# Kernel tuning notes

Measured on AMD Instinct MI355X. Metric: run time of the kernel, lower is better.

The kernel has to match this reference:

```python
import jax, jax.numpy as jnp
import numpy as np

N = 100000
E = 1600000
D_IN = 128
HEADS = 4
C = 16  # hidden // heads
NEG_SLOPE = 0.2


def setup_inputs() -> dict:
    key = jax.random.key(0)
    ks = jax.random.split(key, 8)
    x = jax.random.normal(ks[0], (N, D_IN), dtype=jnp.float32)
    edge_index = jax.random.randint(ks[1], (2, E), 0, N, dtype=jnp.int32)
    s = 1.0 / np.sqrt(D_IN)
    W_l = jax.random.normal(ks[2], (D_IN, HEADS * C), dtype=jnp.float32) * s
    b_l = jnp.zeros((HEADS * C,), dtype=jnp.float32)
    W_r = jax.random.normal(ks[3], (D_IN, HEADS * C), dtype=jnp.float32) * s
    b_r = jnp.zeros((HEADS * C,), dtype=jnp.float32)
    att = jax.random.normal(ks[4], (HEADS, C), dtype=jnp.float32) * (1.0 / np.sqrt(C))
    bias = jnp.zeros((HEADS * C,), dtype=jnp.float32)
    W_head = jax.random.normal(ks[5], (HEADS * C, 1), dtype=jnp.float32) * (1.0 / np.sqrt(HEADS * C))
    b_head = jnp.zeros((1,), dtype=jnp.float32)
    return {"x": x, "edge_index": edge_index, "W_l": W_l, "b_l": b_l,
            "W_r": W_r, "b_r": b_r, "att": att, "bias": bias,
            "W_head": W_head, "b_head": b_head}


def reference(x, edge_index, W_l, b_l, W_r, b_r, att, bias, W_head, b_head):
    # GATv2Conv (PyG semantics, add_self_loops=True, concat=True)
    n = x.shape[0]
    # add self loops
    loops = jnp.arange(n, dtype=edge_index.dtype)
    src = jnp.concatenate([edge_index[0], loops])  # source j
    dst = jnp.concatenate([edge_index[1], loops])  # target i
    # per-node linear projections -> [N, H, C]
    x_l = (x @ W_l + b_l).reshape(n, HEADS, C)
    x_r = (x @ W_r + b_r).reshape(n, HEADS, C)
    # per-edge attention logits: att . LeakyReLU(x_l[j] + x_r[i])
    e = x_l[src] + x_r[dst]                               # [E', H, C]
    e = jnp.where(e >= 0, e, NEG_SLOPE * e)
    logits = jnp.einsum('ehc,hc->eh', e, att)             # [E', H]
    # segment softmax over incoming edges of each target node
    seg_max = jax.ops.segment_max(logits, dst, num_segments=n)  # [N, H]
    expw = jnp.exp(logits - seg_max[dst])
    seg_sum = jax.ops.segment_sum(expw, dst, num_segments=n)
    alpha = expw / seg_sum[dst]                           # [E', H]
    # weighted scatter-aggregate of source messages
    msg = alpha[:, :, None] * x_l[src]                    # [E', H, C]
    out = jax.ops.segment_sum(msg, dst, num_segments=n)   # [N, H, C]
    out = out.reshape(n, HEADS * C) + bias
    # ReLU + Linear head
    h = jax.nn.relu(out)
    return (h @ W_head + b_head).squeeze(-1)              # [N]
```

## Files before the change

### kernel.cpp

```cpp
#include <hip/hip_runtime.h>
#include <hip/hip_bf16.h>
#include <hip/hip_fp16.h>

#define HC 64
#define D_IN 128
#define NEG_SLOPE 0.2f
#define BCAP 8192

using f32x4 = __attribute__((ext_vector_type(4))) float;
using f16x8 = __attribute__((ext_vector_type(8))) _Float16;
using f16x2 = __attribute__((ext_vector_type(2))) _Float16;

__global__ void k_iota(int* __restrict__ p, int n) {
    int i = blockIdx.x * blockDim.x + threadIdx.x;
    if (i < n) p[i] = i * BCAP;
}

__global__ __launch_bounds__(256, 3) void k_proj(
    const float* __restrict__ x,
    const float* __restrict__ Wl, const float* __restrict__ bl,
    const float* __restrict__ Wr, const float* __restrict__ br,
    __half* __restrict__ xlh, float* __restrict__ xr, int N) {
    __shared__ _Float16 sWT[128 * 136];
    const int t = threadIdx.x;
    for (int idx = t; idx < 8192; idx += 256) {
        const int k = idx >> 6;
        const int c = idx & 63;
        sWT[c * 136 + k]        = (_Float16)Wl[idx];
        sWT[(c + 64) * 136 + k] = (_Float16)Wr[idx];
    }
    const int lane = t & 63;
    const int wave = t >> 6;
    const int m = lane & 15;
    const int q = lane >> 4;
    float bfu[8];
#pragma unroll
    for (int ct = 0; ct < 4; ++ct) bfu[ct] = bl[ct * 16 + m];
#pragma unroll
    for (int ct = 0; ct < 4; ++ct) bfu[4 + ct] = br[ct * 16 + m];
    __syncthreads();

    const int ntrip = N >> 5;
    for (int trip = blockIdx.x * 4 + wave; trip < ntrip; trip += gridDim.x * 4) {
        const int i0 = trip << 5;
        f16x8 af[2][4];
#pragma unroll
        for (int tt = 0; tt < 2; ++tt) {
            const float* xrow = x + (size_t)(i0 + tt * 16 + m) * D_IN + q * 8;
#pragma unroll
            for (int kk = 0; kk < 4; ++kk) {
                const float4* p4 = (const float4*)(xrow + kk * 32);
                float4 u = p4[0];
                float4 v = p4[1];
                f16x8 a;
                a[0] = (_Float16)u.x; a[1] = (_Float16)u.y;
                a[2] = (_Float16)u.z; a[3] = (_Float16)u.w;
                a[4] = (_Float16)v.x; a[5] = (_Float16)v.y;
                a[6] = (_Float16)v.z; a[7] = (_Float16)v.w;
                af[tt][kk] = a;
            }
        }
#pragma unroll
        for (int ct = 0; ct < 8; ++ct) {
            const _Float16* bp = &sWT[(ct * 16 + m) * 136 + q * 8];
            f32x4 acc0 = {0.f, 0.f, 0.f, 0.f};
            f32x4 acc1 = {0.f, 0.f, 0.f, 0.f};
#pragma unroll
            for (int kk = 0; kk < 4; ++kk) {
                f16x8 bf = *(const f16x8*)(bp + kk * 32);
                acc0 = __builtin_amdgcn_mfma_f32_16x16x32_f16(af[0][kk], bf, acc0, 0, 0, 0);
                acc1 = __builtin_amdgcn_mfma_f32_16x16x32_f16(af[1][kk], bf, acc1, 0, 0, 0);
            }
            const float bv = bfu[ct];
            if (ct < 4) {
                const int ch = ct * 16 + m;
#pragma unroll
                for (int r = 0; r < 4; ++r) {
                    xlh[(size_t)(i0 + q * 4 + r) * HC + ch]      = __float2half(acc0[r] + bv);
                    xlh[(size_t)(i0 + 16 + q * 4 + r) * HC + ch] = __float2half(acc1[r] + bv);
                }
            } else {
                const int ch = (ct - 4) * 16 + m;
#pragma unroll
                for (int r = 0; r < 4; ++r) {
                    xr[(size_t)(i0 + q * 4 + r) * HC + ch]      = acc0[r] + bv;
                    xr[(size_t)(i0 + 16 + q * 4 + r) * HC + ch] = acc1[r] + bv;
                }
            }
        }
    }
}

__global__ __launch_bounds__(256) void k_scat1(const int* __restrict__ src,
                                               const int* __restrict__ dst, int E,
                                               int* __restrict__ bfill,
                                               unsigned* __restrict__ coarse) {
    __shared__ int h[512], bl[512], cur[512];
    for (int t = threadIdx.x; t < 512; t += 256) { h[t] = 0; cur[t] = 0; }
    __syncthreads();
    const int beg = blockIdx.x * 8192;
    const int end = min(beg + 8192, E);
    for (int p = beg + threadIdx.x; p < end; p += 256)
        atomicAdd(&h[dst[p] >> 8], 1);
    __syncthreads();
    for (int t = threadIdx.x; t < 512; t += 256)
        bl[t] = h[t] ? atomicAdd(&bfill[t], h[t]) : 0;
    __syncthreads();
    for (int p = beg + threadIdx.x; p < end; p += 256) {
        const int d = dst[p];
        const int bin = d >> 8;
        const int r = atomicAdd(&cur[bin], 1);
        coarse[bl[bin] + r] = ((unsigned)src[p] << 8) | (unsigned)(d & 255);
    }
}

__global__ __launch_bounds__(256) void k_sort2(const unsigned* __restrict__ coarse,
                                               const int* __restrict__ bfill,
                                               int* __restrict__ row_off,
                                               int* __restrict__ endo,
                                               int* __restrict__ sorted_src, int N) {
    __shared__ int cnt[256], lds[256];
    const int t = threadIdx.x;
    const int b = blockIdx.x;
    const int eb = b * BCAP;
    const int ee = bfill[b];
    cnt[t] = 0;
    __syncthreads();
    for (int p = eb + t; p < ee; p += 256)
        atomicAdd(&cnt[coarse[p] & 255], 1);
    __syncthreads();
    const int c = cnt[t];
    lds[t] = c;
    __syncthreads();
    for (int o = 1; o < 256; o <<= 1) {
        int v = (t >= o) ? lds[t - o] : 0;
        __syncthreads();
        lds[t] += v;
        __syncthreads();
    }
    const int ex = lds[t] - c;
    const int node = (b << 8) + t;
    if (node < N) {
        row_off[node] = eb + ex;
        endo[node]    = eb + ex + c;
    }
    __syncthreads();
    cnt[t] = ex;
    __syncthreads();
    for (int p = eb + t; p < ee; p += 256) {
        const unsigned e = coarse[p];
        const int r = atomicAdd(&cnt[e & 255], 1);
        sorted_src[eb + r] = (int)(e >> 8);
    }
}

__device__ __forceinline__ float redquad(float v) {
    int a;
    a = __builtin_amdgcn_update_dpp(0, __float_as_int(v), 0xB1, 0xF, 0xF, true);
    v += __int_as_float(a);
    a = __builtin_amdgcn_update_dpp(0, __float_as_int(v), 0x4E, 0xF, 0xF, true);
    v += __int_as_float(a);
    return v;
}

__global__ __launch_bounds__(256) void k_agg(
    const __half* __restrict__ xlh, const float* __restrict__ xr,
    const float* __restrict__ att, const float* __restrict__ bias,
    const float* __restrict__ Wh, const float* __restrict__ bh,
    const int* __restrict__ row_off, const int* __restrict__ endo,
    const int* __restrict__ sorted_src, float* __restrict__ out, int N) {
    const int wave = threadIdx.x >> 6;
    const int lane = threadIdx.x & 63;
    const int i = blockIdx.x * 4 + wave;
    if (i >= N) return;
    const int sl   = lane & 15;
    const int slot = lane >> 4;

    const _Float16* xlhp = (const _Float16*)xlh;
    const float4 attf = *(const float4*)(att + 4 * sl);
    f16x2 attA, attB;
    attA[0] = (_Float16)(attf.x * 1.44269504f);
    attA[1] = (_Float16)(attf.y * 1.44269504f);
    attB[0] = (_Float16)(attf.z * 1.44269504f);
    attB[1] = (_Float16)(attf.w * 1.44269504f);
    const f16x2 c02 = {(_Float16)NEG_SLOPE, (_Float16)NEG_SLOPE};

    const float4 xrf = *(const float4*)(xr + ((size_t)i << 6) + 4 * sl);
    f16x2 xriA, xriB;
    xriA[0] = (_Float16)xrf.x; xriA[1] = (_Float16)xrf.y;
    xriB[0] = (_Float16)xrf.z; xriB[1] = (_Float16)xrf.w;
    const uint2 xliraw = *(const uint2*)(xlhp + ((size_t)i << 6) + 4 * sl);
    const f16x2 xliA = __builtin_bit_cast(f16x2, xliraw.x);
    const f16x2 xliB = __builtin_bit_cast(f16x2, xliraw.y);

    f16x2 vA = xliA + xriA, vB = xliB + xriB;
    vA = __builtin_elementwise_max(vA, vA * c02);
    vB = __builtin_elementwise_max(vB, vB * c02);
    float t0 = redquad(__builtin_amdgcn_fdot2(attB, vB,
                        __builtin_amdgcn_fdot2(attA, vA, 0.f, false), false));
    float pe0 = (slot == 0) ? exp2f(t0) : 0.f;
    float s  = pe0;
    float a0 = pe0 * (float)xliA[0];
    float a1 = pe0 * (float)xliA[1];
    float a2 = pe0 * (float)xliB[0];
    float a3 = pe0 * (float)xliB[1];

    int p = row_off[i];
    const int end = endo[i];

#define EDGE_GROUP(JEXPR, PRED)                                              \
    {                                                                        \
        int jj = (JEXPR);                                                    \
        uint2 raw = *(const uint2*)(xlhp + ((size_t)jj << 6) + 4 * sl);      \
        f16x2 xA = __builtin_bit_cast(f16x2, raw.x);                         \
        f16x2 xB = __builtin_bit_cast(f16x2, raw.y);                         \
        f16x2 wA = xA + xriA, wB = xB + xriB;                                \
        wA = __builtin_elementwise_max(wA, wA * c02);                        \
        wB = __builtin_elementwise_max(wB, wB * c02);                        \
        float tt = redquad(__builtin_amdgcn_fdot2(attB, wB,                  \
                     __builtin_amdgcn_fdot2(attA, wA, 0.f, false), false));  \
        float pe = (PRED) ? exp2f(tt) : 0.f;                                 \
        s += pe;                                                             \
        a0 = fmaf(pe, (float)xA[0], a0);                                     \
        a1 = fmaf(pe, (float)xA[1], a1);                                     \
        a2 = fmaf(pe, (float)xB[0], a2);                                     \
        a3 = fmaf(pe, (float)xB[1], a3);                                     \
    }

    for (; p + 8 <= end; p += 8) {
        int j0 = sorted_src[p + slot];
        int j1 = sorted_src[p + 4 + slot];
        EDGE_GROUP(j0, true)
        EDGE_GROUP(j1, true)
    }
    if (p + 4 <= end) {
        int j0 = sorted_src[p + slot];
        EDGE_GROUP(j0, true)
        p += 4;
    }
    const int rem = end - p;
    if (rem > 0) {
        int idx = p + slot;
        int j0 = sorted_src[(idx < end) ? idx : (end - 1)];
        EDGE_GROUP(j0, slot < rem)
    }
#undef EDGE_GROUP

    s  += __shfl_xor(s, 16);  s  += __shfl_xor(s, 32);
    a0 += __shfl_xor(a0, 16); a0 += __shfl_xor(a0, 32);
    a1 += __shfl_xor(a1, 16); a1 += __shfl_xor(a1, 32);
    a2 += __shfl_xor(a2, 16); a2 += __shfl_xor(a2, 32);
    a3 += __shfl_xor(a3, 16); a3 += __shfl_xor(a3, 32);

    const float4 bi = *(const float4*)(bias + 4 * sl);
    const float4 wh = *(const float4*)(Wh + 4 * sl);
    float y = fmaxf(a0 / s + bi.x, 0.f) * wh.x
            + fmaxf(a1 / s + bi.y, 0.f) * wh.y
            + fmaxf(a2 / s + bi.z, 0.f) * wh.z
            + fmaxf(a3 / s + bi.w, 0.f) * wh.w;
    y += __shfl_xor(y, 1);
    y += __shfl_xor(y, 2);
    y += __shfl_xor(y, 4);
    y += __shfl_xor(y, 8);
    if (lane == 0) out[i] = y + bh[0];
}

extern "C" void kernel_launch(void* const* d_in, const int* in_sizes, int n_in,
                              void* d_out, int out_size, void* d_ws, size_t ws_size,
                              hipStream_t stream) {
    const float* x   = (const float*)d_in[0];
    const int*   ei  = (const int*)d_in[1];
    const float* Wl  = (const float*)d_in[2];
    const float* bl  = (const float*)d_in[3];
    const float* Wr  = (const float*)d_in[4];
    const float* br  = (const float*)d_in[5];
    const float* att = (const float*)d_in[6];
    const float* bias= (const float*)d_in[7];
    const float* Wh  = (const float*)d_in[8];
    const float* bh  = (const float*)d_in[9];
    float* out = (float*)d_out;

    const int N = in_sizes[0] / D_IN;
    const int E = in_sizes[1] / 2;
    const int* src = ei;
    const int* dst = ei + E;
    const int nbkt = (N + 255) / 256;

    auto align = [](size_t v) { return (v + 255) & ~(size_t)255; };
    char* ws = (char*)d_ws;
    size_t off = 0;
    __half* xlh     = (__half*)(ws + off);   off = align(off + (size_t)N * HC * 2);
    float* xr       = (float*)(ws + off);    off = align(off + (size_t)N * HC * 4);
    int*   row_off  = (int*)(ws + off);      off = align(off + (size_t)N * 4);
    int*   endo     = (int*)(ws + off);      off = align(off + (size_t)N * 4);
    int*   bfill    = (int*)(ws + off);      off = align(off + 512 * 4);
    int*   sorted   = (int*)(ws + off);      off = align(off + (size_t)nbkt * BCAP * 4);
    unsigned* coarse= (unsigned*)(ws + off); off = align(off + (size_t)nbkt * BCAP * 4);
    (void)ws_size;

    k_iota<<<2, 256, 0, stream>>>(bfill, 512);

    k_proj<<<782, 256, 0, stream>>>(x, Wl, bl, Wr, br, xlh, xr, N);

    k_scat1<<<(E + 8191) / 8192, 256, 0, stream>>>(src, dst, E, bfill, coarse);
    k_sort2<<<nbkt, 256, 0, stream>>>(coarse, bfill, row_off, endo, sorted, N);

    k_agg<<<(N + 3) / 4, 256, 0, stream>>>(xlh, xr, att, bias, Wh, bh,
                                           row_off, endo, sorted, out, N);
}
```

Baseline: 229.7 us.

## Stage x tiles in LDS for projection, widen agg lanes to 8 channels

The projection kernel now stages a 32-row tile of x into LDS, converted to fp16, once per block, and splits the 8 output column tiles across the 4 waves. Before, each wave loaded its own rows and computed all 8 column tiles. In the aggregation kernel each lane now handles 8 channels with one 16-byte gather, so 8 edges are processed in parallel per wave instead of 4, and the per-edge reduction drops to a single DPP step. The scatter chunk size and the projection grid size also change. These trade extra block-level barriers and more registers per lane for wider memory accesses and more edge parallelism.

```diff
diff --git a/kernel.cpp b/kernel.cpp
--- a/kernel.cpp
+++ b/kernel.cpp
@@ -6,6 +6,7 @@
 #define D_IN 128
 #define NEG_SLOPE 0.2f
 #define BCAP 8192
+#define L2E 1.44269504f
 
 using f32x4 = __attribute__((ext_vector_type(4))) float;
 using f16x8 = __attribute__((ext_vector_type(8))) _Float16;
@@ -22,6 +23,7 @@
     const float* __restrict__ Wr, const float* __restrict__ br,
     __half* __restrict__ xlh, float* __restrict__ xr, int N) {
     __shared__ _Float16 sWT[128 * 136];
+    __shared__ _Float16 sX[32 * 136];
     const int t = threadIdx.x;
     for (int idx = t; idx < 8192; idx += 256) {
         const int k = idx >> 6;
@@ -33,35 +35,35 @@
     const int wave = t >> 6;
     const int m = lane & 15;
     const int q = lane >> 4;
-    float bfu[8];
-#pragma unroll
-    for (int ct = 0; ct < 4; ++ct) bfu[ct] = bl[ct * 16 + m];
-#pragma unroll
-    for (int ct = 0; ct < 4; ++ct) bfu[4 + ct] = br[ct * 16 + m];
+    float bfu[2];
+#pragma unroll
+    for (int cc = 0; cc < 2; ++cc) {
+        const int ct = wave * 2 + cc;
+        const int ch = (ct & 3) * 16 + m;
+        bfu[cc] = (ct < 4) ? bl[ch] : br[ch];
+    }
     __syncthreads();
 
     const int ntrip = N >> 5;
-    for (int trip = blockIdx.x * 4 + wave; trip < ntrip; trip += gridDim.x * 4) {
+    for (int trip = blockIdx.x; trip < ntrip; trip += gridDim.x) {
         const int i0 = trip << 5;
+        for (int c = t; c < 1024; c += 256) {
+            const int r = c >> 5, c4 = c & 31;
+            float4 v = ((const float4*)(x + (size_t)(i0 + r) * D_IN))[c4];
+            _Float16* dp = &sX[r * 136 + c4 * 4];
+            dp[0] = (_Float16)v.x; dp[1] = (_Float16)v.y;
+            dp[2] = (_Float16)v.z; dp[3] = (_Float16)v.w;
+        }
+        __syncthreads();
         f16x8 af[2][4];
 #pragma unroll
-        for (int tt = 0; tt < 2; ++tt) {
-            const float* xrow = x + (size_t)(i0 + tt * 16 + m) * D_IN + q * 8;
-#pragma unroll
-            for (int kk = 0; kk < 4; ++kk) {
-                const float4* p4 = (const float4*)(xrow + kk * 32);
-                float4 u = p4[0];
-                float4 v = p4[1];
-                f16x8 a;
-                a[0] = (_Float16)u.x; a[1] = (_Float16)u.y;
-                a[2] = (_Float16)u.z; a[3] = (_Float16)u.w;
-                a[4] = (_Float16)v.x; a[5] = (_Float16)v.y;
-                a[6] = (_Float16)v.z; a[7] = (_Float16)v.w;
-                af[tt][kk] = a;
-            }
-        }
-#pragma unroll
-        for (int ct = 0; ct < 8; ++ct) {
+        for (int tt = 0; tt < 2; ++tt)
+#pragma unroll
+            for (int kk = 0; kk < 4; ++kk)
+                af[tt][kk] = *(const f16x8*)&sX[(tt * 16 + m) * 136 + kk * 32 + q * 8];
+#pragma unroll
+        for (int cc = 0; cc < 2; ++cc) {
+            const int ct = wave * 2 + cc;
             const _Float16* bp = &sWT[(ct * 16 + m) * 136 + q * 8];
             f32x4 acc0 = {0.f, 0.f, 0.f, 0.f};
             f32x4 acc1 = {0.f, 0.f, 0.f, 0.f};
@@ -71,7 +73,7 @@
                 acc0 = __builtin_amdgcn_mfma_f32_16x16x32_f16(af[0][kk], bf, acc0, 0, 0, 0);
                 acc1 = __builtin_amdgcn_mfma_f32_16x16x32_f16(af[1][kk], bf, acc1, 0, 0, 0);
             }
-            const float bv = bfu[ct];
+            const float bv = bfu[cc];
             if (ct < 4) {
                 const int ch = ct * 16 + m;
 #pragma unroll
@@ -88,6 +90,7 @@
                 }
             }
         }
+        __syncthreads();
     }
 }
 
@@ -98,8 +101,8 @@
     __shared__ int h[512], bl[512], cur[512];
     for (int t = threadIdx.x; t < 512; t += 256) { h[t] = 0; cur[t] = 0; }
     __syncthreads();
-    const int beg = blockIdx.x * 8192;
-    const int end = min(beg + 8192, E);
+    const int beg = blockIdx.x * 4096;
+    const int end = min(beg + 4096, E);
     for (int p = beg + threadIdx.x; p < end; p += 256)
         atomicAdd(&h[dst[p] >> 8], 1);
     __syncthreads();
@@ -154,13 +157,9 @@
     }
 }
 
-__device__ __forceinline__ float redquad(float v) {
-    int a;
-    a = __builtin_amdgcn_update_dpp(0, __float_as_int(v), 0xB1, 0xF, 0xF, true);
-    v += __int_as_float(a);
-    a = __builtin_amdgcn_update_dpp(0, __float_as_int(v), 0x4E, 0xF, 0xF, true);
-    v += __int_as_float(a);
-    return v;
+__device__ __forceinline__ float redpair(float v) {
+    int a = __builtin_amdgcn_update_dpp(0, __float_as_int(v), 0xB1, 0xF, 0xF, true);
+    return v + __int_as_float(a);
 }
 
 __global__ __launch_bounds__(256) void k_agg(
@@ -173,95 +172,123 @@
     const int lane = threadIdx.x & 63;
     const int i = blockIdx.x * 4 + wave;
     if (i >= N) return;
-    const int sl   = lane & 15;
-    const int slot = lane >> 4;
+    const int sub  = lane & 7;
+    const int slot = lane >> 3;
 
     const _Float16* xlhp = (const _Float16*)xlh;
-    const float4 attf = *(const float4*)(att + 4 * sl);
-    f16x2 attA, attB;
-    attA[0] = (_Float16)(attf.x * 1.44269504f);
-    attA[1] = (_Float16)(attf.y * 1.44269504f);
-    attB[0] = (_Float16)(attf.z * 1.44269504f);
-    attB[1] = (_Float16)(attf.w * 1.44269504f);
+    const float4 atA = *(const float4*)(att + 8 * sub);
+    const float4 atB = *(const float4*)(att + 8 * sub + 4);
+    f16x2 at[4];
+    at[0][0] = (_Float16)(atA.x * L2E); at[0][1] = (_Float16)(atA.y * L2E);
+    at[1][0] = (_Float16)(atA.z * L2E); at[1][1] = (_Float16)(atA.w * L2E);
+    at[2][0] = (_Float16)(atB.x * L2E); at[2][1] = (_Float16)(atB.y * L2E);
+    at[3][0] = (_Float16)(atB.z * L2E); at[3][1] = (_Float16)(atB.w * L2E);
     const f16x2 c02 = {(_Float16)NEG_SLOPE, (_Float16)NEG_SLOPE};
 
-    const float4 xrf = *(const float4*)(xr + ((size_t)i << 6) + 4 * sl);
-    f16x2 xriA, xriB;
-    xriA[0] = (_Float16)xrf.x; xriA[1] = (_Float16)xrf.y;
-    xriB[0] = (_Float16)xrf.z; xriB[1] = (_Float16)xrf.w;
-    const uint2 xliraw = *(const uint2*)(xlhp + ((size_t)i << 6) + 4 * sl);
-    const f16x2 xliA = __builtin_bit_cast(f16x2, xliraw.x);
-    const f16x2 xliB = __builtin_bit_cast(f16x2, xliraw.y);
-
-    f16x2 vA = xliA + xriA, vB = xliB + xriB;
-    vA = __builtin_elementwise_max(vA, vA * c02);
-    vB = __builtin_elementwise_max(vB, vB * c02);
-    float t0 = redquad(__builtin_amdgcn_fdot2(attB, vB,
-                        __builtin_amdgcn_fdot2(attA, vA, 0.f, false), false));
-    float pe0 = (slot == 0) ? exp2f(t0) : 0.f;
-    float s  = pe0;
-    float a0 = pe0 * (float)xliA[0];
-    float a1 = pe0 * (float)xliA[1];
-    float a2 = pe0 * (float)xliB[0];
-    float a3 = pe0 * (float)xliB[1];
+    const float4 xrA = *(const float4*)(xr + ((size_t)i << 6) + 8 * sub);
+    const float4 xrB = *(const float4*)(xr + ((size_t)i << 6) + 8 * sub + 4);
+    f16x2 xri[4];
+    xri[0][0] = (_Float16)xrA.x; xri[0][1] = (_Float16)xrA.y;
+    xri[1][0] = (_Float16)xrA.z; xri[1][1] = (_Float16)xrA.w;
+    xri[2][0] = (_Float16)xrB.x; xri[2][1] = (_Float16)xrB.y;
+    xri[3][0] = (_Float16)xrB.z; xri[3][1] = (_Float16)xrB.w;
+
+    const uint4 xliraw = *(const uint4*)(xlhp + ((size_t)i << 6) + 8 * sub);
+    f16x2 xli[4];
+    xli[0] = __builtin_bit_cast(f16x2, xliraw.x);
+    xli[1] = __builtin_bit_cast(f16x2, xliraw.y);
+    xli[2] = __builtin_bit_cast(f16x2, xliraw.z);
+    xli[3] = __builtin_bit_cast(f16x2, xliraw.w);
+
+    float t0 = 0.f;
+#pragma unroll
+    for (int c = 0; c < 4; ++c) {
+        f16x2 w = xli[c] + xri[c];
+        w = __builtin_elementwise_max(w, w * c02);
+        t0 = __builtin_amdgcn_fdot2(at[c], w, t0, false);
+    }
+    t0 = redpair(t0);
+    const float pe0 = (slot == 0) ? exp2f(t0) : 0.f;
+    float s = pe0;
+    float a[8];
+#pragma unroll
+    for (int c = 0; c < 4; ++c) {
+        a[2 * c]     = pe0 * (float)xli[c][0];
+        a[2 * c + 1] = pe0 * (float)xli[c][1];
+    }
 
     int p = row_off[i];
     const int end = endo[i];
 
 #define EDGE_GROUP(JEXPR, PRED)                                              \
     {                                                                        \
-        int jj = (JEXPR);                                                    \
-        uint2 raw = *(const uint2*)(xlhp + ((size_t)jj << 6) + 4 * sl);      \
-        f16x2 xA = __builtin_bit_cast(f16x2, raw.x);                         \
-        f16x2 xB = __builtin_bit_cast(f16x2, raw.y);                         \
-        f16x2 wA = xA + xriA, wB = xB + xriB;                                \
-        wA = __builtin_elementwise_max(wA, wA * c02);                        \
-        wB = __builtin_elementwise_max(wB, wB * c02);                        \
-        float tt = redquad(__builtin_amdgcn_fdot2(attB, wB,                  \
-                     __builtin_amdgcn_fdot2(attA, wA, 0.f, false), false));  \
-        float pe = (PRED) ? exp2f(tt) : 0.f;                                 \
+        const int jj = (JEXPR);                                              \
+        const uint4 raw = *(const uint4*)(xlhp + ((size_t)jj << 6) + 8 * sub);\
+        f16x2 xv[4];                                                         \
+        xv[0] = __builtin_bit_cast(f16x2, raw.x);                            \
+        xv[1] = __builtin_bit_cast(f16x2, raw.y);                            \
+        xv[2] = __builtin_bit_cast(f16x2, raw.z);                            \
+        xv[3] = __builtin_bit_cast(f16x2, raw.w);                            \
+        float tt = 0.f;                                                      \
+        _Pragma("unroll")                                                    \
+        for (int c = 0; c < 4; ++c) {                                        \
+            f16x2 w = xv[c] + xri[c];                                        \
+            w = __builtin_elementwise_max(w, w * c02);                       \
+            tt = __builtin_amdgcn_fdot2(at[c], w, tt, false);                \
+        }                                                                    \
+        tt = redpair(tt);                                                    \
+        const float pe = (PRED) ? exp2f(tt) : 0.f;                           \
         s += pe;                                                             \
-        a0 = fmaf(pe, (float)xA[0], a0);                                     \
-        a1 = fmaf(pe, (float)xA[1], a1);                                     \
-        a2 = fmaf(pe, (float)xB[0], a2);                                     \
-        a3 = fmaf(pe, (float)xB[1], a3);                                     \
-    }
-
-    for (; p + 8 <= end; p += 8) {
-        int j0 = sorted_src[p + slot];
-        int j1 = sorted_src[p + 4 + slot];
+        _Pragma("unroll")                                                    \
+        for (int c = 0; c < 4; ++c) {                                        \
+            a[2 * c]     = fmaf(pe, (float)xv[c][0], a[2 * c]);              \
+            a[2 * c + 1] = fmaf(pe, (float)xv[c][1], a[2 * c + 1]);          \
+        }                                                                    \
+    }
+
+    for (; p + 16 <= end; p += 16) {
+        const int j0 = sorted_src[p + slot];
+        const int j1 = sorted_src[p + 8 + slot];
         EDGE_GROUP(j0, true)
         EDGE_GROUP(j1, true)
     }
-    if (p + 4 <= end) {
-        int j0 = sorted_src[p + slot];
+    if (p + 8 <= end) {
+        const int j0 = sorted_src[p + slot];
         EDGE_GROUP(j0, true)
-        p += 4;
+        p += 8;
     }
     const int rem = end - p;
     if (rem > 0) {
-        int idx = p + slot;
-        int j0 = sorted_src[(idx < end) ? idx : (end - 1)];
+        const int idx = p + slot;
+        const int j0 = sorted_src[(idx < end) ? idx : (end - 1)];
         EDGE_GROUP(j0, slot < rem)
     }
 #undef EDGE_GROUP
 
-    s  += __shfl_xor(s, 16);  s  += __shfl_xor(s, 32);
-    a0 += __shfl_xor(a0, 16); a0 += __shfl_xor(a0, 32);
-    a1 += __shfl_xor(a1, 16); a1 += __shfl_xor(a1, 32);
-    a2 += __shfl_xor(a2, 16); a2 += __shfl_xor(a2, 32);
-    a3 += __shfl_xor(a3, 16); a3 += __shfl_xor(a3, 32);
-
-    const float4 bi = *(const float4*)(bias + 4 * sl);
-    const float4 wh = *(const float4*)(Wh + 4 * sl);
-    float y = fmaxf(a0 / s + bi.x, 0.f) * wh.x
-            + fmaxf(a1 / s + bi.y, 0.f) * wh.y
-            + fmaxf(a2 / s + bi.z, 0.f) * wh.z
-            + fmaxf(a3 / s + bi.w, 0.f) * wh.w;
+    s += __shfl_xor(s, 8);  s += __shfl_xor(s, 16);  s += __shfl_xor(s, 32);
+#pragma unroll
+    for (int c = 0; c < 8; ++c) {
+        a[c] += __shfl_xor(a[c], 8);
+        a[c] += __shfl_xor(a[c], 16);
+        a[c] += __shfl_xor(a[c], 32);
+    }
+
+    const float4 biA = *(const float4*)(bias + 8 * sub);
+    const float4 biB = *(const float4*)(bias + 8 * sub + 4);
+    const float4 whA = *(const float4*)(Wh + 8 * sub);
+    const float4 whB = *(const float4*)(Wh + 8 * sub + 4);
+    const float inv = 1.f / s;
+    float y = fmaxf(a[0] * inv + biA.x, 0.f) * whA.x
+            + fmaxf(a[1] * inv + biA.y, 0.f) * whA.y
+            + fmaxf(a[2] * inv + biA.z, 0.f) * whA.z
+            + fmaxf(a[3] * inv + biA.w, 0.f) * whA.w
+            + fmaxf(a[4] * inv + biB.x, 0.f) * whB.x
+            + fmaxf(a[5] * inv + biB.y, 0.f) * whB.y
+            + fmaxf(a[6] * inv + biB.z, 0.f) * whB.z
+            + fmaxf(a[7] * inv + biB.w, 0.f) * whB.w;
     y += __shfl_xor(y, 1);
     y += __shfl_xor(y, 2);
     y += __shfl_xor(y, 4);
-    y += __shfl_xor(y, 8);
     if (lane == 0) out[i] = y + bh[0];
 }
 
@@ -300,9 +327,9 @@
 
     k_iota<<<2, 256, 0, stream>>>(bfill, 512);
 
-    k_proj<<<782, 256, 0, stream>>>(x, Wl, bl, Wr, br, xlh, xr, N);
-
-    k_scat1<<<(E + 8191) / 8192, 256, 0, stream>>>(src, dst, E, bfill, coarse);
+    k_proj<<<1024, 256, 0, stream>>>(x, Wl, bl, Wr, br, xlh, xr, N);
+
+    k_scat1<<<(E + 4095) / 4096, 256, 0, stream>>>(src, dst, E, bfill, coarse);
     k_sort2<<<nbkt, 256, 0, stream>>>(coarse, bfill, row_off, endo, sorted, N);
 
     k_agg<<<(N + 3) / 4, 256, 0, stream>>>(xlh, xr, att, bias, Wh, bh,
```

Result: no change. 226.1 us (-1.5%).
